# Optimization experiments

Measured on AMD Instinct MI355X. Metric: run time of the kernel, lower is better.

Reference implementation:

```python
import jax, jax.numpy as jnp
import numpy as np

# --- static config (matches init_kwargs) ---
B, S, DIM = 1, 2048, 1024
H, G, DK, DV = 16, 4, 64, 64
HPG = H // G
L, D, LSEL, NSEL, W = 32, 16, 64, 16, 512
NCMP = (S - L) // D + 1            # number of compressed blocks over full prefill
J = S // LSEL                      # number of selection blocks
GH = 32                            # gate hidden
NEG = -1e30


def rope(x, pos):
    # x: [B, S, N, Dh]; llama-style half rotation
    Dh = x.shape[-1]
    inv = 1.0 / (10000.0 ** (np.arange(0, Dh, 2) / Dh))
    ang = pos[:, None] * inv[None, :]                      # [S, Dh/2]
    cos = jnp.asarray(np.cos(ang), jnp.float32)[None, :, None, :]
    sin = jnp.asarray(np.sin(ang), jnp.float32)[None, :, None, :]
    x1, x2 = jnp.split(x, 2, axis=-1)
    return jnp.concatenate([x1 * cos - x2 * sin, x2 * cos + x1 * sin], axis=-1)


def masked_softmax(s, m):
    p = jax.nn.softmax(jnp.where(m, s, NEG), axis=-1)
    # rows with no visible keys produce 0 output (empty attention)
    return jnp.where(jnp.any(m, axis=-1, keepdims=True), p, 0.0)


def setup_inputs() -> dict:
    key = jax.random.key(0)
    ks = jax.random.split(key, 12)
    def w(k, shape, fan):
        return jax.random.normal(k, shape, jnp.float32) / np.sqrt(fan)
    return {
        'x': jax.random.normal(ks[0], (B, S, DIM), jnp.float32),
        'W_Q': w(ks[1], (DIM, H * DK), DIM),
        'W_K_sel': w(ks[2], (DIM, G * DK), DIM),
        'W_V_sel': w(ks[3], (DIM, G * DV), DIM),
        'W_K_win': w(ks[4], (DIM, G * DK), DIM),
        'W_V_win': w(ks[5], (DIM, G * DV), DIM),
        'W_K_cmp': w(ks[6], (DIM, G * DK), DIM),
        'W_V_cmp': w(ks[7], (DIM, G * DV), DIM),
        'W_out': w(ks[8], (H * DV, DIM), H * DV),
        'gate_w1': w(ks[9], (DK, GH), DK),
        'gate_b1': jnp.zeros((GH,), jnp.float32),
        'gate_w2': 0.1 * jax.random.normal(ks[10], (GH, 3), jnp.float32),
        'gate_b2': jnp.zeros((3,), jnp.float32),
    }


def reference(x, W_Q, W_K_sel, W_V_sel, W_K_win, W_V_win, W_K_cmp, W_V_cmp,
              W_out, gate_w1, gate_b1, gate_w2, gate_b2):
    pos = np.arange(S)
    s_ = np.arange(S)
    scale = 1.0 / np.sqrt(DK)

    Q = rope((x @ W_Q).reshape(B, S, H, DK), pos).reshape(B, S, G, HPG, DK)

    def proj_kv(Wk, Wv):
        K = rope((x @ Wk).reshape(B, S, G, DK), pos).transpose(0, 2, 1, 3)  # [B,G,S,Dk]
        V = (x @ Wv).reshape(B, S, G, DV).transpose(0, 2, 1, 3)            # [B,G,S,Dv]
        return K, V

    K_sel, V_sel = proj_kv(W_K_sel, W_V_sel)
    K_win, V_win = proj_kv(W_K_win, W_V_win)
    K_cr, V_cr = proj_kv(W_K_cmp, W_V_cmp)

    # --- compressed branch: avg-pool (len L, stride D) of roped K / raw V ---
    bidx = np.arange(NCMP)[:, None] * D + np.arange(L)[None, :]   # [NCMP, L]
    K_cmp = K_cr[:, :, bidx].mean(axis=3)                         # [B,G,NCMP,Dk]
    V_cmp = V_cr[:, :, bidx].mean(axis=3)
    vis_c = (np.arange(NCMP)[None, :] * D + L) <= (s_[:, None] + 1)  # block fully in past
    sc_c = jnp.einsum('bsghd,bgcd->bsghc', Q, K_cmp) * scale
    p_cmp = masked_softmax(sc_c, jnp.asarray(vis_c)[None, :, None, None, :])
    O_cmp = jnp.einsum('bsghc,bgce->bsghe', p_cmp, V_cmp)

    # --- map compressed probs -> selection-block scores (overlap fractions) ---
    i0 = np.arange(NCMP)[:, None] * D
    j0 = np.arange(J)[None, :] * LSEL
    ov = np.maximum(0, np.minimum(i0 + L, j0 + LSEL) - np.maximum(i0, j0)) / L
    p_grp = jnp.einsum('bsghc,cj->bsgj', p_cmp, jnp.asarray(ov, np.float32))  # sum over heads in group

    vis_j = (np.arange(J)[None, :] * LSEL) <= s_[:, None]
    forced = (np.arange(J)[None, :] == 0) | (np.arange(J)[None, :] == (s_ // LSEL)[:, None])
    score = jnp.where(jnp.asarray(vis_j)[None, :, None, :], p_grp, NEG)
    score = jnp.where(jnp.asarray(forced)[None, :, None, :], 1e9, score)  # force block 0 + current block
    topj = jax.lax.top_k(score, NSEL)[1]                                   # [B,S,G,NSEL]
    blk = jax.nn.one_hot(topj, J, dtype=jnp.float32).sum(axis=-2) > 0      # [B,S,G,J]

    tok2blk = np.repeat(np.arange(J), LSEL)[:S]
    causal = s_[:, None] >= s_[None, :]                                    # u <= t
    sel_mask = blk[:, :, :, tok2blk] & jnp.asarray(causal)[None, :, None, :]  # [B,S,G,S]
    sc_s = jnp.einsum('bsghd,bgud->bsghu', Q, K_sel) * scale
    O_sel = jnp.einsum('bsghu,bgue->bsghe',
                       masked_softmax(sc_s, sel_mask[:, :, :, None, :]), V_sel)

    # --- sliding window branch ---
    win_mask = causal & (s_[None, :] > s_[:, None] - W)
    sc_w = jnp.einsum('bsghd,bgud->bsghu', Q, K_win) * scale
    O_win = jnp.einsum('bsghu,bgue->bsghe',
                       masked_softmax(sc_w, jnp.asarray(win_mask)[None, :, None, None, :]), V_win)

    # --- gating MLP on head-pooled query per group ---
    gl = jax.nn.silu(Q.mean(axis=3) @ gate_w1 + gate_b1) @ gate_w2 + gate_b2  # [B,S,G,3]
    pg = jax.nn.softmax(gl, axis=-1)
    t2 = jax.lax.top_k(gl, 2)[0]
    peaked = (t2[..., 0] - t2[..., 1]) > 50.0
    gates = jnp.where(peaked[..., None],
                      jax.nn.one_hot(jnp.argmax(gl, axis=-1), 3, dtype=gl.dtype), pg)

    O = (gates[..., 0, None, None] * O_cmp
         + gates[..., 1, None, None] * O_sel
         + gates[..., 2, None, None] * O_win)          # [B,S,G,h,Dv]
    return O.reshape(B, S, H * DV) @ W_out
```

## Files before the change

### kernel.cpp

```cpp
#include <hip/hip_runtime.h>
#include <math.h>

#define S 2048
#define DIM 1024
#define H 16
#define G 4
#define HPG 4
#define DK 64
#define DV 64
#define NCMP 127
#define JBLK 32
#define NSEL 16
#define WWIN 512
#define GH 32
#define SCL2 0.18033688011112042f

typedef __attribute__((ext_vector_type(8))) __bf16 bf16x8;
typedef __attribute__((ext_vector_type(4))) float f32x4;

__device__ __forceinline__ unsigned short f2bf(float f) {
  unsigned u = __float_as_uint(f);
  unsigned r = (u + 0x7FFFu + ((u >> 16) & 1u)) >> 16;
  return (unsigned short)r;
}

__device__ __forceinline__ unsigned short f2bf_hw(float f) {
  __bf16 b = (__bf16)f;
  return *(unsigned short*)&b;
}

__device__ __forceinline__ float bf2f(unsigned short u) {
  return __uint_as_float((unsigned)u << 16);
}

__device__ __forceinline__ f32x4 mfma16(bf16x8 a, bf16x8 b, f32x4 c) {
  return __builtin_amdgcn_mfma_f32_16x16x32_bf16(a, b, c, 0, 0, 0);
}

__global__ void rope_table(float* __restrict__ cosT, float* __restrict__ sinT) {
  int idx = blockIdx.x * blockDim.x + threadIdx.x;
  if (idx >= S * 32) return;
  int s = idx >> 5, i = idx & 31;
  double inv = pow(10000.0, -2.0 * (double)i / 64.0);
  double ang = (double)s * inv;
  cosT[idx] = (float)cos(ang);
  sinT[idx] = (float)sin(ang);
}

__device__ __forceinline__ void gemm_body_k(const float* __restrict__ A,
                                            const float* __restrict__ B,
                                            float* __restrict__ C,
                                            int N, int K, int bm, int bn,
                                            int kS, int kE,
                                            float* As , float* Bs ) {
  int tid = threadIdx.x;
  int tr = tid >> 4, tc = tid & 15;
  float acc[4][4] = {{0.f}};
  int arow = tid >> 2;
  int kba = (tid & 3) << 3;
  int brow = tid >> 4;
  int bcol = (tid & 15) << 2;
  const float* Ab = A + (size_t)(bm * 64) * K;
  const float* Bb = B + bn * 64;

  float4 a0 = *(const float4*)(Ab + (size_t)arow * K + kS + kba);
  float4 a1 = *(const float4*)(Ab + (size_t)arow * K + kS + kba + 4);
  float4 b0 = *(const float4*)(Bb + (size_t)(kS + brow) * N + bcol);
  float4 b1 = *(const float4*)(Bb + (size_t)(kS + brow + 16) * N + bcol);

  for (int k0 = kS; k0 < kE; k0 += 32) {
    __syncthreads();
    {
      float av[8] = {a0.x, a0.y, a0.z, a0.w, a1.x, a1.y, a1.z, a1.w};
#pragma unroll
      for (int i = 0; i < 8; ++i) {
        int k = kba + i;
        As[k * 64 + (arow ^ (((k >> 3) & 3) << 3))] = av[i];
      }
      *(float4*)&Bs[brow * 64 + bcol] = b0;
      *(float4*)&Bs[(brow + 16) * 64 + bcol] = b1;
    }
    __syncthreads();
    if (k0 + 32 < kE) {
      a0 = *(const float4*)(Ab + (size_t)arow * K + k0 + 32 + kba);
      a1 = *(const float4*)(Ab + (size_t)arow * K + k0 + 32 + kba + 4);
      b0 = *(const float4*)(Bb + (size_t)(k0 + 32 + brow) * N + bcol);
      b1 = *(const float4*)(Bb + (size_t)(k0 + 32 + brow + 16) * N + bcol);
    }
#pragma unroll
    for (int kk = 0; kk < 32; ++kk) {
      float4 a = *(const float4*)&As[kk * 64 + ((tr << 2) ^ (((kk >> 3) & 3) << 3))];
      float4 b = *(const float4*)&Bs[kk * 64 + (tc << 2)];
      acc[0][0] += a.x * b.x; acc[0][1] += a.x * b.y; acc[0][2] += a.x * b.z; acc[0][3] += a.x * b.w;
      acc[1][0] += a.y * b.x; acc[1][1] += a.y * b.y; acc[1][2] += a.y * b.z; acc[1][3] += a.y * b.w;
      acc[2][0] += a.z * b.x; acc[2][1] += a.z * b.y; acc[2][2] += a.z * b.z; acc[2][3] += a.z * b.w;
      acc[3][0] += a.w * b.x; acc[3][1] += a.w * b.y; acc[3][2] += a.w * b.z; acc[3][3] += a.w * b.w;
    }
  }
  for (int i = 0; i < 4; ++i)
    for (int jj = 0; jj < 4; ++jj)
      C[(size_t)(bm * 64 + (tr << 2) + i) * N + bn * 64 + (tc << 2) + jj] = acc[i][jj];
}

__device__ __forceinline__ void proj_body(
    const unsigned short* __restrict__ xb, const unsigned short* __restrict__ Wt,
    const float* __restrict__ cosT, const float* __restrict__ sinT,
    unsigned short* __restrict__ Kb_s, unsigned short* __restrict__ Vt_s,
    unsigned short* __restrict__ Kb_w, unsigned short* __restrict__ Vt_w,
    unsigned short* __restrict__ Vt_c,
    int s0, int g, int mat, unsigned short* xs, unsigned short* ws) {
  int tid = threadIdx.x, w = tid >> 6, lane = tid & 63;
  int l15 = lane & 15, lg = lane >> 4;
  int rswz = (l15 & 7) << 3;
  bool isV = (mat == 1) || (mat == 3) || (mat == 4);
  const unsigned short* wt = Wt + ((size_t)mat * 256 + g * 64) * 1024;

  f32x4 acc[4];
#pragma unroll
  for (int nt = 0; nt < 4; ++nt) acc[nt] = (f32x4){0.f, 0.f, 0.f, 0.f};

  for (int k0 = 0; k0 < DIM; k0 += 64) {
#pragma unroll
    for (int e = 0; e < 2; ++e) {
      int flat = tid + e * 256;
      int row = flat >> 3, cc = flat & 7;
      int dsti = row * 64 + ((cc ^ (row & 7)) << 3);
      *(float4*)&xs[dsti] = *(const float4*)(xb + (size_t)(s0 + row) * DIM + k0 + cc * 8);
      *(float4*)&ws[dsti] = *(const float4*)(wt + (size_t)row * DIM + k0 + cc * 8);
    }
    __syncthreads();
    const unsigned short* aP = isV ? ws : xs;
    const unsigned short* bP = isV ? xs : ws;
    int arow = w * 16 + l15;
    bf16x8 af[2];
#pragma unroll
    for (int kc = 0; kc < 2; ++kc)
      af[kc] = *(const bf16x8*)&aP[(arow * 64 + kc * 32 + lg * 8) ^ rswz];
#pragma unroll
    for (int nt = 0; nt < 4; ++nt) {
      int brow = nt * 16 + l15;
      bf16x8 b0 = *(const bf16x8*)&bP[(brow * 64 + lg * 8) ^ rswz];
      bf16x8 b1 = *(const bf16x8*)&bP[(brow * 64 + 32 + lg * 8) ^ rswz];
      acc[nt] = mfma16(af[0], b0, acc[nt]);
      acc[nt] = mfma16(af[1], b1, acc[nt]);
    }
    __syncthreads();
  }

  if (!isV) {
    unsigned short* Kb = (mat == 0) ? Kb_s : Kb_w;
#pragma unroll
    for (int rr = 0; rr < 4; ++rr) {
      int tok = s0 + w * 16 + lg * 4 + rr;
#pragma unroll
      for (int p = 0; p < 2; ++p) {
        int i = p * 16 + l15;
        float c = cosT[tok * 32 + i], sn = sinT[tok * 32 + i];
        float x1 = acc[p][rr], x2 = acc[p + 2][rr];
        Kb[((size_t)g * S + tok) * 64 + i] = f2bf(x1 * c - x2 * sn);
        Kb[((size_t)g * S + tok) * 64 + i + 32] = f2bf(x2 * c + x1 * sn);
      }
    }
  } else {
    unsigned short* Vt = (mat == 1) ? Vt_s : (mat == 3) ? Vt_w : Vt_c;
#pragma unroll
    for (int rr = 0; rr < 4; ++rr) {
      int col = w * 16 + lg * 4 + rr;
#pragma unroll
      for (int nt = 0; nt < 4; ++nt) {
        int tok = s0 + nt * 16 + l15;
        Vt[((size_t)g * 64 + col) * S + tok] = f2bf(acc[nt][rr]);
      }
    }
  }
}

__global__ __launch_bounds__(256) void qk_proj(
    const float* __restrict__ x, const float* __restrict__ W_Q,
    const float* __restrict__ W_Kc, float* __restrict__ Pq, float* __restrict__ Pk,
    const unsigned short* __restrict__ xb, const unsigned short* __restrict__ Wt,
    const float* __restrict__ cosT, const float* __restrict__ sinT,
    unsigned short* __restrict__ Kb_s, unsigned short* __restrict__ Vt_s,
    unsigned short* __restrict__ Kb_w, unsigned short* __restrict__ Vt_w,
    unsigned short* __restrict__ Vt_c) {
  __shared__ __align__(16) float lds_f[4096];
  int bid = blockIdx.x;
  int r = bid % 3;
  if (r < 2) {
    int gid = (bid / 3) * 2 + r;
    int z = gid / 640;
    int rem = gid % 640;
    int ct = rem % 20;
    int bm = rem / 20;
    int kS = z * 512, kE = kS + 512;
    float* As = lds_f;
    float* Bs = lds_f + 2048;
    if (ct < 16)
      gemm_body_k(x, W_Q, Pq + (size_t)z * S * 1024, 1024, DIM, bm, ct, kS, kE, As, Bs);
    else
      gemm_body_k(x, W_Kc, Pk + (size_t)z * S * 256, 256, DIM, bm, ct - 16, kS, kE, As, Bs);
  } else {
    int pid = bid / 3;
    int s0b = pid % 32;
    int g = (pid / 32) % 4;
    int mat = pid / 128;
    unsigned short* xs = (unsigned short*)lds_f;
    unsigned short* ws = xs + 4096;
    proj_body(xb, Wt, cosT, sinT, Kb_s, Vt_s, Kb_w, Vt_w, Vt_c, s0b * 64, g, mat,
              xs, ws);
  }
}

__global__ __launch_bounds__(256) void reduce_rope(
    const float* __restrict__ Pq, const float* __restrict__ Pk,
    const float* __restrict__ cosT, const float* __restrict__ sinT,
    float* __restrict__ Qb, unsigned short* __restrict__ Qbf,
    float* __restrict__ Kcr) {
  int idx = blockIdx.x * 256 + threadIdx.x;
  const int NQ = S * H * 32;
  if (idx < NQ) {
    int i = idx & 31;
    int rest = idx >> 5;
    int h = rest & 15;
    int s = rest >> 4;
    size_t base = (size_t)s * 1024 + h * 64 + i;
    float a1 = Pq[base] + Pq[(size_t)S * 1024 + base];
    float a2 = Pq[base + 32] + Pq[(size_t)S * 1024 + base + 32];
    float c = cosT[s * 32 + i], sn = sinT[s * 32 + i];
    float q1 = a1 * c - a2 * sn, q2 = a2 * c + a1 * sn;
    Qb[base] = q1;
    Qb[base + 32] = q2;
    Qbf[base] = f2bf(q1);
    Qbf[base + 32] = f2bf(q2);
  } else {
    int j = idx - NQ;
    if (j >= S * G * 32) return;
    int i = j & 31;
    int rest = j >> 5;
    int g = rest & 3;
    int s = rest >> 2;
    size_t base = (size_t)s * 256 + g * 64 + i;
    float a1 = Pk[base] + Pk[(size_t)S * 256 + base];
    float a2 = Pk[base + 32] + Pk[(size_t)S * 256 + base + 32];
    float c = cosT[s * 32 + i], sn = sinT[s * 32 + i];
    Kcr[base] = a1 * c - a2 * sn;
    Kcr[base + 32] = a2 * c + a1 * sn;
  }
}

__global__ __launch_bounds__(256) void fconv(const float* __restrict__ a,
                                             unsigned short* __restrict__ b) {
  int idx = (blockIdx.x * 256 + threadIdx.x) * 8;
  float4 x = *(const float4*)&a[idx];
  float4 y = *(const float4*)&a[idx + 4];
  union { unsigned short us[8]; float4 f4; } t;
  t.us[0] = f2bf(x.x); t.us[1] = f2bf(x.y); t.us[2] = f2bf(x.z); t.us[3] = f2bf(x.w);
  t.us[4] = f2bf(y.x); t.us[5] = f2bf(y.y); t.us[6] = f2bf(y.z); t.us[7] = f2bf(y.w);
  *(float4*)&b[idx] = t.f4;
}

__global__ __launch_bounds__(256) void wtrans(const float* __restrict__ W0,
                                              const float* __restrict__ W1,
                                              const float* __restrict__ W2,
                                              const float* __restrict__ W3,
                                              const float* __restrict__ W4,
                                              unsigned short* __restrict__ Wt) {
  __shared__ float t[64][65];
  int k0 = blockIdx.x * 64;
  int n0 = blockIdx.y * 64;
  int m = blockIdx.z;
  const float* W = (m == 0) ? W0 : (m == 1) ? W1 : (m == 2) ? W2 : (m == 3) ? W3 : W4;
  int tid = threadIdx.x;
  int rr = tid >> 4, c4 = (tid & 15) * 4;
#pragma unroll
  for (int e = 0; e < 4; ++e) {
    int row = rr + e * 16;
    float4 v = *(const float4*)(W + (size_t)(k0 + row) * 256 + n0 + c4);
    t[c4 + 0][row] = v.x;
    t[c4 + 1][row] = v.y;
    t[c4 + 2][row] = v.z;
    t[c4 + 3][row] = v.w;
  }
  __syncthreads();
#pragma unroll
  for (int e = 0; e < 2; ++e) {
    int flat = tid + e * 256;
    int col = flat >> 3, kc = (flat & 7) * 8;
    union { unsigned short us[8]; float4 f4; } u;
#pragma unroll
    for (int i = 0; i < 8; ++i) u.us[i] = f2bf(t[col][kc + i]);
    *(float4*)(Wt + ((size_t)m * 256 + n0 + col) * 1024 + k0 + kc) = u.f4;
  }
}

__global__ __launch_bounds__(256) void wtrans_o(const float* __restrict__ W,
                                                unsigned short* __restrict__ Wt) {
  __shared__ float t[64][65];
  int k0 = blockIdx.x * 64;
  int n0 = blockIdx.y * 64;
  int tid = threadIdx.x;
  int rr = tid >> 4, c4 = (tid & 15) * 4;
#pragma unroll
  for (int e = 0; e < 4; ++e) {
    int row = rr + e * 16;
    float4 v = *(const float4*)(W + (size_t)(k0 + row) * 1024 + n0 + c4);
    t[c4 + 0][row] = v.x;
    t[c4 + 1][row] = v.y;
    t[c4 + 2][row] = v.z;
    t[c4 + 3][row] = v.w;
  }
  __syncthreads();
#pragma unroll
  for (int e = 0; e < 2; ++e) {
    int flat = tid + e * 256;
    int col = flat >> 3, kc = (flat & 7) * 8;
    union { unsigned short us[8]; float4 f4; } u;
#pragma unroll
    for (int i = 0; i < 8; ++i) u.us[i] = f2bf(t[col][kc + i]);
    *(float4*)(Wt + (size_t)(n0 + col) * 1024 + k0 + kc) = u.f4;
  }
}

__global__ __launch_bounds__(256) void gemm_out(const unsigned short* __restrict__ Ob,
                                                const unsigned short* __restrict__ Wt,
                                                float* __restrict__ out) {
  __shared__ unsigned short xs[64 * 64];
  __shared__ unsigned short ws[64 * 64];
  int s0 = blockIdx.x * 64;
  int n0 = blockIdx.y * 64;
  int tid = threadIdx.x, w = tid >> 6, lane = tid & 63;
  int l15 = lane & 15, lg = lane >> 4;
  int rswz = (l15 & 7) << 3;

  f32x4 acc[4];
#pragma unroll
  for (int nt = 0; nt < 4; ++nt) acc[nt] = (f32x4){0.f, 0.f, 0.f, 0.f};

  for (int k0 = 0; k0 < DIM; k0 += 64) {
#pragma unroll
    for (int e = 0; e < 2; ++e) {
      int flat = tid + e * 256;
      int row = flat >> 3, cc = flat & 7;
      int dsti = row * 64 + ((cc ^ (row & 7)) << 3);
      *(float4*)&xs[dsti] = *(const float4*)(Ob + (size_t)(s0 + row) * DIM + k0 + cc * 8);
      *(float4*)&ws[dsti] = *(const float4*)(Wt + (size_t)(n0 + row) * DIM + k0 + cc * 8);
    }
    __syncthreads();
    int arow = w * 16 + l15;
    bf16x8 af0 = *(const bf16x8*)&xs[(arow * 64 + lg * 8) ^ rswz];
    bf16x8 af1 = *(const bf16x8*)&xs[(arow * 64 + 32 + lg * 8) ^ rswz];
#pragma unroll
    for (int nt = 0; nt < 4; ++nt) {
      int brow = nt * 16 + l15;
      bf16x8 b0 = *(const bf16x8*)&ws[(brow * 64 + lg * 8) ^ rswz];
      bf16x8 b1 = *(const bf16x8*)&ws[(brow * 64 + 32 + lg * 8) ^ rswz];
      acc[nt] = mfma16(af0, b0, acc[nt]);
      acc[nt] = mfma16(af1, b1, acc[nt]);
    }
    __syncthreads();
  }

#pragma unroll
  for (int nt = 0; nt < 4; ++nt)
#pragma unroll
    for (int rr = 0; rr < 4; ++rr)
      out[(size_t)(s0 + w * 16 + lg * 4 + rr) * 1024 + n0 + nt * 16 + l15] =
          acc[nt][rr];
}

__global__ void pool_cmp(const float* __restrict__ Kcr,
                         const unsigned short* __restrict__ Vtc,
                         float* __restrict__ Kc, float* __restrict__ Vc) {
  int c = blockIdx.x, g = blockIdx.y, d = threadIdx.x;
  float sk = 0.f, sv = 0.f;
  const unsigned short* vrow = Vtc + ((size_t)g * 64 + d) * S + c * 16;
  for (int l = 0; l < 32; ++l) {
    sk += Kcr[(size_t)((c * 16 + l) * G + g) * 64 + d];
    sv += bf2f(vrow[l]);
  }
  Kc[(size_t)(g * NCMP + c) * 64 + d] = sk * (1.f / 32.f);
  Vc[(size_t)(g * NCMP + c) * 64 + d] = sv * (1.f / 32.f);
}

__device__ __forceinline__ void cmp_body(const float* __restrict__ Q,
                                         const float* __restrict__ Kc,
                                         const float* __restrict__ Vc,
                                         float* __restrict__ Ocmp,
                                         unsigned int* __restrict__ selm,
                                         int s, int g,
                                         float* q4 , float* sc ,
                                         float* pg ) {
  int tid = threadIdx.x;
  int nvis = (s >= 31) ? (((s - 31) >> 4) + 1) : 0;
  {
    int h = tid >> 6, d = tid & 63;
    q4[h * 64 + d] = Q[(size_t)(s * H + g * HPG + h) * 64 + d];
  }
  __syncthreads();

  if (tid < 128) {
    int c = tid;
    if (c < nvis) {
      float a0 = 0.f, a1 = 0.f, a2 = 0.f, a3 = 0.f;
      const float* kr = &Kc[(size_t)(g * NCMP + c) * 64];
#pragma unroll 4
      for (int kk = 0; kk < 16; ++kk) {
        float4 kv = *(const float4*)&kr[kk * 4];
        float4 q0 = *(const float4*)&q4[0 * 64 + kk * 4];
        float4 q1 = *(const float4*)&q4[1 * 64 + kk * 4];
        float4 q2 = *(const float4*)&q4[2 * 64 + kk * 4];
        float4 q3 = *(const float4*)&q4[3 * 64 + kk * 4];
        a0 += q0.x * kv.x + q0.y * kv.y + q0.z * kv.z + q0.w * kv.w;
        a1 += q1.x * kv.x + q1.y * kv.y + q1.z * kv.z + q1.w * kv.w;
        a2 += q2.x * kv.x + q2.y * kv.y + q2.z * kv.z + q2.w * kv.w;
        a3 += q3.x * kv.x + q3.y * kv.y + q3.z * kv.z + q3.w * kv.w;
      }
      sc[0 * 128 + c] = a0 * 0.125f;
      sc[1 * 128 + c] = a1 * 0.125f;
      sc[2 * 128 + c] = a2 * 0.125f;
      sc[3 * 128 + c] = a3 * 0.125f;
    } else {
      sc[0 * 128 + c] = -INFINITY;
      sc[1 * 128 + c] = -INFINITY;
      sc[2 * 128 + c] = -INFINITY;
      sc[3 * 128 + c] = -INFINITY;
    }
  }
  __syncthreads();

  int w = tid >> 6, lane = tid & 63;
  {
    float v0 = sc[w * 128 + lane];
    float v1 = (lane + 64 < NCMP) ? sc[w * 128 + lane + 64] : -INFINITY;
    float m = fmaxf(v0, v1);
    for (int off = 32; off; off >>= 1) m = fmaxf(m, __shfl_xor(m, off));
    float e0 = (m > -INFINITY && v0 > -INFINITY) ? expf(v0 - m) : 0.f;
    float e1 = (m > -INFINITY && v1 > -INFINITY) ? expf(v1 - m) : 0.f;
    float sum = e0 + e1;
    for (int off = 32; off; off >>= 1) sum += __shfl_xor(sum, off);
    float inv = (sum > 0.f) ? 1.f / sum : 0.f;
    sc[w * 128 + lane] = e0 * inv;
    if (lane + 64 < NCMP) sc[w * 128 + lane + 64] = e1 * inv;
    if (lane == 63) sc[w * 128 + 127] = 0.f;
  }
  __syncthreads();

  {
    int h = tid >> 6, d = tid & 63;
    float o = 0.f;
#pragma unroll 4
    for (int c = 0; c < nvis; ++c)
      o += sc[h * 128 + c] * Vc[(size_t)(g * NCMP + c) * 64 + d];
    Ocmp[(size_t)(s * H + g * HPG + h) * 64 + d] = o;
  }

  if (tid < JBLK) {
    int j = tid;
    float a = 0.f;
#pragma unroll
    for (int h = 0; h < 4; ++h) {
      const float* row = &sc[h * 128];
      float v = row[4 * j] + row[4 * j + 1] + row[4 * j + 2] + 0.5f * row[4 * j + 3];
      if (j > 0) v += 0.5f * row[4 * j - 1];
      a += v;
    }
    pg[j] = a;
  }
  __syncthreads();

  if (tid < 64) {
    int j = tid & 31;
    int cur = s >> 6;
    float v = (j * 64 <= s) ? pg[j] : -1e30f;
    if (j == 0 || j == cur) v = 1e9f;
    unsigned int mask = 0;
#pragma unroll 1
    for (int n = 0; n < NSEL; ++n) {
      float bv = v;
      int bj = j;
#pragma unroll
      for (int off = 1; off < 32; off <<= 1) {
        float ov = __shfl_xor(bv, off);
        int oj = __shfl_xor(bj, off);
        if (ov > bv || (ov == bv && oj < bj)) { bv = ov; bj = oj; }
      }
      mask |= 1u << bj;
      if (j == bj) v = -INFINITY;
    }
    if (tid == 0) selm[(size_t)s * G + g] = mask;
  }
}

template <int MODE>
__device__ __forceinline__ void attn_body(
    const unsigned short* __restrict__ Qbf, const unsigned short* __restrict__ Kb,
    const unsigned short* __restrict__ Vtb, const unsigned int* __restrict__ selm,
    float* __restrict__ O, int t0, int g,
    unsigned short* Kl, unsigned short* Vt, unsigned short* Pl,
    unsigned int* sel_l, int* blist, int* nB_p) {
  int tid = threadIdx.x;
  int w = tid >> 6, lane = tid & 63;
  int l15 = lane & 15, lg = lane >> 4;
  int rswz = (l15 & 7) << 3;
  int jdiag = t0 >> 6;

  if (MODE == 0 && tid < 16) sel_l[tid] = selm[(t0 + tid) * G + g];
  __syncthreads();
  if (tid == 0) {
    int n = 0;
    if (MODE == 0) {
      unsigned int un = 0;
      for (int i = 0; i < 16; ++i) un |= sel_l[i];
      for (int j = 0; j <= jdiag; ++j)
        if ((un >> j) & 1u) blist[n++] = j;
    } else {
      int lo = t0 - (WWIN - 1);
      int j0 = (lo > 0) ? (lo >> 6) : 0;
      for (int j = j0; j <= jdiag; ++j) blist[n++] = j;
    }
    *nB_p = n;
  }
  __syncthreads();
  int nB = *nB_p;

  int tok = t0 + l15;
  bf16x8 qf[2];
  {
    const unsigned short* qb = Qbf + ((size_t)tok * H + g * HPG + w) * 64;
    qf[0] = *(const bf16x8*)(qb + lg * 8);
    qf[1] = *(const bf16x8*)(qb + 32 + lg * 8);
  }

  float mrun = -INFINITY, lrun = 0.f;
  f32x4 oacc[4];
#pragma unroll
  for (int dt = 0; dt < 4; ++dt) oacc[dt] = (f32x4){0.f, 0.f, 0.f, 0.f};

  for (int b = 0; b < nB; ++b) {
    int j = blist[b];
    int ku = j * 64;

    {
      const unsigned short* src = Kb + ((size_t)g * S + ku) * 64;
#pragma unroll
      for (int c2 = 0; c2 < 2; ++c2) {
        int chunk = tid + c2 * 256;
        int key = chunk >> 3, cc = chunk & 7;
        *(float4*)&Kl[key * 64 + ((cc ^ (key & 7)) << 3)] =
            *(const float4*)(src + chunk * 8);
      }
#pragma unroll
      for (int c2 = 0; c2 < 2; ++c2) {
        int chunk = tid + c2 * 256;
        int dim = chunk >> 3, cc = chunk & 7;
        *(float4*)&Vt[dim * 64 + ((cc ^ (dim & 7)) << 3)] =
            *(const float4*)(Vtb + ((size_t)g * 64 + dim) * S + ku + cc * 8);
      }
    }
    __syncthreads();

    f32x4 sf[4];
#pragma unroll
    for (int kt = 0; kt < 4; ++kt) sf[kt] = (f32x4){0.f, 0.f, 0.f, 0.f};
#pragma unroll
    for (int kt = 0; kt < 4; ++kt) {
      int krow = kt * 16 + l15;
      bf16x8 kf0 = *(const bf16x8*)&Kl[(krow * 64 + lg * 8) ^ rswz];
      bf16x8 kf1 = *(const bf16x8*)&Kl[(krow * 64 + 32 + lg * 8) ^ rswz];
      sf[kt] = mfma16(kf0, qf[0], sf[kt]);
      sf[kt] = mfma16(kf1, qf[1], sf[kt]);
    }

    bool bsel = true;
    if (MODE == 0) bsel = ((sel_l[l15] >> j) & 1u) != 0;
    float sv2[4][4];
    if (j == jdiag) {
#pragma unroll
      for (int kt = 0; kt < 4; ++kt)
#pragma unroll
        for (int rr = 0; rr < 4; ++rr) {
          int u = ku + kt * 16 + lg * 4 + rr;
          sv2[kt][rr] = (u <= tok) ? sf[kt][rr] * SCL2 : -INFINITY;
        }
    } else if (MODE == 1 && (ku + WWIN <= t0 + 15)) {
#pragma unroll
      for (int kt = 0; kt < 4; ++kt)
#pragma unroll
        for (int rr = 0; rr < 4; ++rr) {
          int u = ku + kt * 16 + lg * 4 + rr;
          sv2[kt][rr] = (u + WWIN > tok) ? sf[kt][rr] * SCL2 : -INFINITY;
        }
    } else {
#pragma unroll
      for (int kt = 0; kt < 4; ++kt)
#pragma unroll
        for (int rr = 0; rr < 4; ++rr) sv2[kt][rr] = sf[kt][rr] * SCL2;
    }

    float pmax = -INFINITY;
#pragma unroll
    for (int kt = 0; kt < 4; ++kt)
#pragma unroll
      for (int rr = 0; rr < 4; ++rr) pmax = fmaxf(pmax, sv2[kt][rr]);
    pmax = fmaxf(pmax, __shfl_xor(pmax, 16));
    pmax = fmaxf(pmax, __shfl_xor(pmax, 32));
    if (MODE == 0 && !bsel) pmax = -INFINITY;

    if (__any(pmax > mrun)) {
      float mnew = fmaxf(mrun, pmax);
      float mc = (mnew == -INFINITY) ? 0.f : mnew;
      float fac = exp2f(mrun - mc);
      mrun = mnew;
      lrun *= fac;
#pragma unroll
      for (int dt = 0; dt < 4; ++dt)
#pragma unroll
        for (int rr = 0; rr < 4; ++rr) oacc[dt][rr] *= fac;
    }
    float mcb = (MODE == 0 && !bsel) ? INFINITY
                                     : ((mrun == -INFINITY) ? 0.f : mrun);

    float psum = 0.f;
    unsigned short pb[16];
#pragma unroll
    for (int kt = 0; kt < 4; ++kt)
#pragma unroll
      for (int rr = 0; rr < 4; ++rr) {
        float e = exp2f(sv2[kt][rr] - mcb);
        psum += e;
        pb[kt * 4 + rr] = f2bf_hw(e);
      }
    psum += __shfl_xor(psum, 16);
    psum += __shfl_xor(psum, 32);
    lrun += psum;

    {
      unsigned short* pw = Pl + w * 1024;
#pragma unroll
      for (int kt = 0; kt < 4; ++kt) {
        int idx = (l15 * 64 + kt * 16 + lg * 4) ^ rswz;
        unsigned int lo = (unsigned)pb[kt * 4] | ((unsigned)pb[kt * 4 + 1] << 16);
        unsigned int hi = (unsigned)pb[kt * 4 + 2] | ((unsigned)pb[kt * 4 + 3] << 16);
        *(uint2*)&pw[idx] = make_uint2(lo, hi);
      }
    }

#pragma unroll
    for (int kc = 0; kc < 2; ++kc) {
      bf16x8 pf = *(const bf16x8*)&Pl[w * 1024 + ((l15 * 64 + kc * 32 + lg * 8) ^ rswz)];
#pragma unroll
      for (int dt = 0; dt < 4; ++dt) {
        bf16x8 vf = *(const bf16x8*)&Vt[((dt * 16 + l15) * 64 + kc * 32 + lg * 8) ^ rswz];
        oacc[dt] = mfma16(vf, pf, oacc[dt]);
      }
    }
    __syncthreads();
  }

  {
    float inv = (lrun > 0.f) ? 1.f / lrun : 0.f;
    float* ob = O + ((size_t)tok * H + g * HPG + w) * 64;
#pragma unroll
    for (int dt = 0; dt < 4; ++dt) {
      float4 v;
      v.x = oacc[dt][0] * inv;
      v.y = oacc[dt][1] * inv;
      v.z = oacc[dt][2] * inv;
      v.w = oacc[dt][3] * inv;
      *(float4*)(ob + dt * 16 + lg * 4) = v;
    }
  }
}

__global__ __launch_bounds__(256) void cmp_win(
    const float* __restrict__ Qb, const float* __restrict__ Kc,
    const float* __restrict__ Vc, float* __restrict__ Ocmp,
    unsigned int* __restrict__ selm, const unsigned short* __restrict__ Qbf,
    const unsigned short* __restrict__ Kbw, const unsigned short* __restrict__ Vtw,
    float* __restrict__ Owin) {
  __shared__ __align__(16) unsigned char ldsb[24832];
  int bid = blockIdx.x;
  if (bid % 17 != 16) {
    int cid = (bid / 17) * 16 + (bid % 17);
    int s = cid >> 2, g = cid & 3;
    float* q4 = (float*)ldsb;
    float* sc = q4 + 256;
    float* pg = sc + 512;
    cmp_body(Qb, Kc, Vc, Ocmp, selm, s, g, q4, sc, pg);
  } else {
    int pid = bid / 17;
    int t0 = (pid & 127) * 16;
    int g = pid >> 7;
    unsigned short* Kl = (unsigned short*)ldsb;
    unsigned short* Vt = Kl + 4096;
    unsigned short* Pl = Vt + 4096;
    int* blist = (int*)(Pl + 4096);
    int* nB_p = blist + JBLK;
    attn_body<1>(Qbf, Kbw, Vtw, nullptr, Owin, t0, g, Kl, Vt, Pl, nullptr, blist,
                 nB_p);
  }
}

__global__ __launch_bounds__(256) void attn_sel(
    const unsigned short* __restrict__ Qbf, const unsigned short* __restrict__ Kbs,
    const unsigned short* __restrict__ Vts, const unsigned int* __restrict__ selm,
    float* __restrict__ Osel) {
  __shared__ unsigned short Kl[4096];
  __shared__ unsigned short Vt[4096];
  __shared__ unsigned short Pl[4096];
  __shared__ unsigned int sel_l[16];
  __shared__ int blist[JBLK];
  __shared__ int nB_s;
  int t0 = blockIdx.x * 16;
  int g = blockIdx.y;
  attn_body<0>(Qbf, Kbs, Vts, selm, Osel, t0, g, Kl, Vt, Pl, sel_l, blist, &nB_s);
}

__global__ void gate_kernel(const float* __restrict__ Q, const float* __restrict__ w1,
                            const float* __restrict__ b1, const float* __restrict__ w2,
                            const float* __restrict__ b2, float* __restrict__ gates) {
  int idx = blockIdx.x * blockDim.x + threadIdx.x;
  if (idx >= S * G) return;
  int s = idx >> 2, g = idx & 3;
  float qm[64];
#pragma unroll
  for (int d = 0; d < 64; ++d) {
    float a = 0.f;
    for (int hp = 0; hp < HPG; ++hp) a += Q[(size_t)(s * H + g * HPG + hp) * 64 + d];
    qm[d] = a * 0.25f;
  }
  float gl[3] = {b2[0], b2[1], b2[2]};
  for (int j = 0; j < GH; ++j) {
    float z = b1[j];
    for (int d = 0; d < 64; ++d) z += qm[d] * w1[d * GH + j];
    float sl = z / (1.f + expf(-z));
    gl[0] += sl * w2[j * 3 + 0];
    gl[1] += sl * w2[j * 3 + 1];
    gl[2] += sl * w2[j * 3 + 2];
  }
  float m = fmaxf(gl[0], fmaxf(gl[1], gl[2]));
  float e0 = expf(gl[0] - m), e1 = expf(gl[1] - m), e2 = expf(gl[2] - m);
  float inv = 1.f / (e0 + e1 + e2);
  float p0 = e0 * inv, p1 = e1 * inv, p2 = e2 * inv;
  int am = (gl[0] >= gl[1] && gl[0] >= gl[2]) ? 0 : ((gl[1] >= gl[2]) ? 1 : 2);
  float t1 = (am == 0) ? fmaxf(gl[1], gl[2]) : ((am == 1) ? fmaxf(gl[0], gl[2]) : fmaxf(gl[0], gl[1]));
  if (m - t1 > 50.f) {
    p0 = (am == 0) ? 1.f : 0.f;
    p1 = (am == 1) ? 1.f : 0.f;
    p2 = (am == 2) ? 1.f : 0.f;
  }
  gates[idx * 3 + 0] = p0;
  gates[idx * 3 + 1] = p1;
  gates[idx * 3 + 2] = p2;
}

__global__ void combine(const float* __restrict__ Oc, const float* __restrict__ Os,
                        const float* __restrict__ Ow, const float* __restrict__ gates,
                        unsigned short* __restrict__ Ob) {
  int idx = blockIdx.x * blockDim.x + threadIdx.x;
  if (idx >= S * H * DV) return;
  int h = (idx >> 6) & 15;
  int s = idx >> 10;
  int g = h >> 2;
  const float* gp = &gates[(size_t)(s * G + g) * 3];
  Ob[idx] = f2bf(gp[0] * Oc[idx] + gp[1] * Os[idx] + gp[2] * Ow[idx]);
}

extern "C" void kernel_launch(void* const* d_in, const int* in_sizes, int n_in,
                              void* d_out, int out_size, void* d_ws, size_t ws_size,
                              hipStream_t stream) {
  const float* x = (const float*)d_in[0];
  const float* W_Q = (const float*)d_in[1];
  const float* W_K_sel = (const float*)d_in[2];
  const float* W_V_sel = (const float*)d_in[3];
  const float* W_K_win = (const float*)d_in[4];
  const float* W_V_win = (const float*)d_in[5];
  const float* W_K_cmp = (const float*)d_in[6];
  const float* W_V_cmp = (const float*)d_in[7];
  const float* W_out = (const float*)d_in[8];
  const float* gw1 = (const float*)d_in[9];
  const float* gb1 = (const float*)d_in[10];
  const float* gw2 = (const float*)d_in[11];
  const float* gb2 = (const float*)d_in[12];

  float* w = (float*)d_ws;
  float* cosT = w;  w += S * 32;
  float* sinT = w;  w += S * 32;
  float* Qb   = w;  w += S * H * DK;
  float* Kcr  = w;  w += S * G * DK;
  float* Kc   = w;  w += G * NCMP * DK;
  float* Vc   = w;  w += G * NCMP * DV;
  float* Ocmp = w;  w += S * H * DV;
  float* Osel = w;  w += S * H * DV;
  float* Owin = w;  w += S * H * DV;
  float* gates= w;  w += S * G * 3;
  unsigned int* selm = (unsigned int*)w;  w += S * G;
  unsigned short* Kbf_s = (unsigned short*)w;  w += (size_t)G * S * 64 / 2;
  unsigned short* Kbf_w = (unsigned short*)w;  w += (size_t)G * S * 64 / 2;
  unsigned short* Vt_s  = (unsigned short*)w;  w += (size_t)G * S * 64 / 2;
  unsigned short* Vt_w  = (unsigned short*)w;  w += (size_t)G * S * 64 / 2;
  unsigned short* Vt_c  = (unsigned short*)w;  w += (size_t)G * S * 64 / 2;
  unsigned short* Qbf   = (unsigned short*)w;  w += (size_t)S * H * 64 / 2;
  unsigned short* xb    = (unsigned short*)w;  w += (size_t)S * DIM / 2;
  unsigned short* Wt    = (unsigned short*)w;  w += (size_t)5 * 256 * DIM / 2;
  unsigned short* Ob    = (unsigned short*)w;  w += (size_t)S * H * DV / 2;
  unsigned short* WtO   = (unsigned short*)w;  w += (size_t)DIM * DIM / 2;

  float* Pq = Ocmp;
  float* Pk = Owin;

  rope_table<<<(S * 32 + 255) / 256, 256, 0, stream>>>(cosT, sinT);
  fconv<<<(S * DIM) / 2048, 256, 0, stream>>>(x, xb);
  wtrans<<<dim3(DIM / 64, 4, 5), 256, 0, stream>>>(W_K_sel, W_V_sel, W_K_win,
                                                   W_V_win, W_V_cmp, Wt);
  wtrans_o<<<dim3(DIM / 64, DIM / 64), 256, 0, stream>>>(W_out, WtO);

  qk_proj<<<1920, 256, 0, stream>>>(x, W_Q, W_K_cmp, Pq, Pk, xb, Wt, cosT, sinT,
                                    Kbf_s, Vt_s, Kbf_w, Vt_w, Vt_c);
  reduce_rope<<<(S * (H + G) * 32) / 256, 256, 0, stream>>>(Pq, Pk, cosT, sinT,
                                                            Qb, Qbf, Kcr);

  pool_cmp<<<dim3(NCMP, G), 64, 0, stream>>>(Kcr, Vt_c, Kc, Vc);

  cmp_win<<<8704, 256, 0, stream>>>(Qb, Kc, Vc, Ocmp, selm, Qbf, Kbf_w, Vt_w, Owin);
  attn_sel<<<dim3(S / 16, G), 256, 0, stream>>>(Qbf, Kbf_s, Vt_s, selm, Osel);

  gate_kernel<<<(S * G + 255) / 256, 256, 0, stream>>>(Qb, gw1, gb1, gw2, gb2, gates);
  combine<<<(S * H * DV + 255) / 256, 256, 0, stream>>>(Ocmp, Osel, Owin, gates, Ob);

  gemm_out<<<dim3(S / 64, DIM / 64), 256, 0, stream>>>(Ob, WtO, (float*)d_out);
}
```

Baseline: 328.6 us.

## Merge prep kernels, fuse pooling with gating, regroup attention launches

Folds the rope table, activation conversion and both weight transposes into one prep launch with block-range dispatch. Compressed-KV pooling and the gating MLP now share one post_reduce launch. The compressed attention gets its own launch, and selection and window attention are merged into one 3D launch instead of interleaving window work with compressed blocks. The aim is fewer launches and better balance between attention branches, at the cost of losing overlap between compressed and window work within a single launch.

```diff
diff --git a/kernel.cpp b/kernel.cpp
--- a/kernel.cpp
+++ b/kernel.cpp
@@ -37,14 +37,82 @@
   return __builtin_amdgcn_mfma_f32_16x16x32_bf16(a, b, c, 0, 0, 0);
 }
 
-__global__ void rope_table(float* __restrict__ cosT, float* __restrict__ sinT) {
-  int idx = blockIdx.x * blockDim.x + threadIdx.x;
-  if (idx >= S * 32) return;
-  int s = idx >> 5, i = idx & 31;
-  double inv = pow(10000.0, -2.0 * (double)i / 64.0);
-  double ang = (double)s * inv;
-  cosT[idx] = (float)cos(ang);
-  sinT[idx] = (float)sin(ang);
+__global__ __launch_bounds__(256) void prep(
+    const float* __restrict__ x, const float* __restrict__ W0,
+    const float* __restrict__ W1, const float* __restrict__ W2,
+    const float* __restrict__ W3, const float* __restrict__ W4,
+    const float* __restrict__ W_out, float* __restrict__ cosT,
+    float* __restrict__ sinT, unsigned short* __restrict__ xb,
+    unsigned short* __restrict__ Wt, unsigned short* __restrict__ WtO) {
+  __shared__ float t[64 * 65];
+  int bid = blockIdx.x, tid = threadIdx.x;
+  if (bid < 256) {
+    int idx = bid * 256 + tid;
+    int s = idx >> 5, i = idx & 31;
+    double inv = pow(10000.0, -2.0 * (double)i / 64.0);
+    double ang = (double)s * inv;
+    cosT[idx] = (float)cos(ang);
+    sinT[idx] = (float)sin(ang);
+  } else if (bid < 1280) {
+    int idx = ((bid - 256) * 256 + tid) * 8;
+    float4 a = *(const float4*)&x[idx];
+    float4 b = *(const float4*)&x[idx + 4];
+    union { unsigned short us[8]; float4 f4; } u;
+    u.us[0] = f2bf(a.x); u.us[1] = f2bf(a.y); u.us[2] = f2bf(a.z); u.us[3] = f2bf(a.w);
+    u.us[4] = f2bf(b.x); u.us[5] = f2bf(b.y); u.us[6] = f2bf(b.z); u.us[7] = f2bf(b.w);
+    *(float4*)&xb[idx] = u.f4;
+  } else if (bid < 1600) {
+    int p = bid - 1280;
+    int m = p / 64;
+    int rem = p % 64;
+    int k0 = (rem & 15) * 64;
+    int n0 = (rem >> 4) * 64;
+    const float* W = (m == 0) ? W0 : (m == 1) ? W1 : (m == 2) ? W2 : (m == 3) ? W3 : W4;
+    int rr = tid >> 4, c4 = (tid & 15) * 4;
+#pragma unroll
+    for (int e = 0; e < 4; ++e) {
+      int row = rr + e * 16;
+      float4 v = *(const float4*)(W + (size_t)(k0 + row) * 256 + n0 + c4);
+      t[(c4 + 0) * 65 + row] = v.x;
+      t[(c4 + 1) * 65 + row] = v.y;
+      t[(c4 + 2) * 65 + row] = v.z;
+      t[(c4 + 3) * 65 + row] = v.w;
+    }
+    __syncthreads();
+#pragma unroll
+    for (int e = 0; e < 2; ++e) {
+      int flat = tid + e * 256;
+      int col = flat >> 3, kc = (flat & 7) * 8;
+      union { unsigned short us[8]; float4 f4; } u;
+#pragma unroll
+      for (int i = 0; i < 8; ++i) u.us[i] = f2bf(t[col * 65 + kc + i]);
+      *(float4*)(Wt + ((size_t)m * 256 + n0 + col) * 1024 + k0 + kc) = u.f4;
+    }
+  } else {
+    int p = bid - 1600;
+    int k0 = (p & 15) * 64;
+    int n0 = (p >> 4) * 64;
+    int rr = tid >> 4, c4 = (tid & 15) * 4;
+#pragma unroll
+    for (int e = 0; e < 4; ++e) {
+      int row = rr + e * 16;
+      float4 v = *(const float4*)(W_out + (size_t)(k0 + row) * 1024 + n0 + c4);
+      t[(c4 + 0) * 65 + row] = v.x;
+      t[(c4 + 1) * 65 + row] = v.y;
+      t[(c4 + 2) * 65 + row] = v.z;
+      t[(c4 + 3) * 65 + row] = v.w;
+    }
+    __syncthreads();
+#pragma unroll
+    for (int e = 0; e < 2; ++e) {
+      int flat = tid + e * 256;
+      int col = flat >> 3, kc = (flat & 7) * 8;
+      union { unsigned short us[8]; float4 f4; } u;
+#pragma unroll
+      for (int i = 0; i < 8; ++i) u.us[i] = f2bf(t[col * 65 + kc + i]);
+      *(float4*)(WtO + (size_t)(n0 + col) * 1024 + k0 + kc) = u.f4;
+    }
+  }
 }
 
 __device__ __forceinline__ void gemm_body_k(const float* __restrict__ A,
@@ -248,138 +316,61 @@
   }
 }
 
-__global__ __launch_bounds__(256) void fconv(const float* __restrict__ a,
-                                             unsigned short* __restrict__ b) {
-  int idx = (blockIdx.x * 256 + threadIdx.x) * 8;
-  float4 x = *(const float4*)&a[idx];
-  float4 y = *(const float4*)&a[idx + 4];
-  union { unsigned short us[8]; float4 f4; } t;
-  t.us[0] = f2bf(x.x); t.us[1] = f2bf(x.y); t.us[2] = f2bf(x.z); t.us[3] = f2bf(x.w);
-  t.us[4] = f2bf(y.x); t.us[5] = f2bf(y.y); t.us[6] = f2bf(y.z); t.us[7] = f2bf(y.w);
-  *(float4*)&b[idx] = t.f4;
-}
-
-__global__ __launch_bounds__(256) void wtrans(const float* __restrict__ W0,
-                                              const float* __restrict__ W1,
-                                              const float* __restrict__ W2,
-                                              const float* __restrict__ W3,
-                                              const float* __restrict__ W4,
-                                              unsigned short* __restrict__ Wt) {
-  __shared__ float t[64][65];
-  int k0 = blockIdx.x * 64;
-  int n0 = blockIdx.y * 64;
-  int m = blockIdx.z;
-  const float* W = (m == 0) ? W0 : (m == 1) ? W1 : (m == 2) ? W2 : (m == 3) ? W3 : W4;
-  int tid = threadIdx.x;
-  int rr = tid >> 4, c4 = (tid & 15) * 4;
-#pragma unroll
-  for (int e = 0; e < 4; ++e) {
-    int row = rr + e * 16;
-    float4 v = *(const float4*)(W + (size_t)(k0 + row) * 256 + n0 + c4);
-    t[c4 + 0][row] = v.x;
-    t[c4 + 1][row] = v.y;
-    t[c4 + 2][row] = v.z;
-    t[c4 + 3][row] = v.w;
-  }
-  __syncthreads();
-#pragma unroll
-  for (int e = 0; e < 2; ++e) {
-    int flat = tid + e * 256;
-    int col = flat >> 3, kc = (flat & 7) * 8;
-    union { unsigned short us[8]; float4 f4; } u;
-#pragma unroll
-    for (int i = 0; i < 8; ++i) u.us[i] = f2bf(t[col][kc + i]);
-    *(float4*)(Wt + ((size_t)m * 256 + n0 + col) * 1024 + k0 + kc) = u.f4;
-  }
-}
-
-__global__ __launch_bounds__(256) void wtrans_o(const float* __restrict__ W,
-                                                unsigned short* __restrict__ Wt) {
-  __shared__ float t[64][65];
-  int k0 = blockIdx.x * 64;
-  int n0 = blockIdx.y * 64;
-  int tid = threadIdx.x;
-  int rr = tid >> 4, c4 = (tid & 15) * 4;
-#pragma unroll
-  for (int e = 0; e < 4; ++e) {
-    int row = rr + e * 16;
-    float4 v = *(const float4*)(W + (size_t)(k0 + row) * 1024 + n0 + c4);
-    t[c4 + 0][row] = v.x;
-    t[c4 + 1][row] = v.y;
-    t[c4 + 2][row] = v.z;
-    t[c4 + 3][row] = v.w;
-  }
-  __syncthreads();
-#pragma unroll
-  for (int e = 0; e < 2; ++e) {
-    int flat = tid + e * 256;
-    int col = flat >> 3, kc = (flat & 7) * 8;
-    union { unsigned short us[8]; float4 f4; } u;
-#pragma unroll
-    for (int i = 0; i < 8; ++i) u.us[i] = f2bf(t[col][kc + i]);
-    *(float4*)(Wt + (size_t)(n0 + col) * 1024 + k0 + kc) = u.f4;
-  }
-}
-
-__global__ __launch_bounds__(256) void gemm_out(const unsigned short* __restrict__ Ob,
-                                                const unsigned short* __restrict__ Wt,
-                                                float* __restrict__ out) {
-  __shared__ unsigned short xs[64 * 64];
-  __shared__ unsigned short ws[64 * 64];
-  int s0 = blockIdx.x * 64;
-  int n0 = blockIdx.y * 64;
-  int tid = threadIdx.x, w = tid >> 6, lane = tid & 63;
-  int l15 = lane & 15, lg = lane >> 4;
-  int rswz = (l15 & 7) << 3;
-
-  f32x4 acc[4];
-#pragma unroll
-  for (int nt = 0; nt < 4; ++nt) acc[nt] = (f32x4){0.f, 0.f, 0.f, 0.f};
-
-  for (int k0 = 0; k0 < DIM; k0 += 64) {
-#pragma unroll
-    for (int e = 0; e < 2; ++e) {
-      int flat = tid + e * 256;
-      int row = flat >> 3, cc = flat & 7;
-      int dsti = row * 64 + ((cc ^ (row & 7)) << 3);
-      *(float4*)&xs[dsti] = *(const float4*)(Ob + (size_t)(s0 + row) * DIM + k0 + cc * 8);
-      *(float4*)&ws[dsti] = *(const float4*)(Wt + (size_t)(n0 + row) * DIM + k0 + cc * 8);
-    }
-    __syncthreads();
-    int arow = w * 16 + l15;
-    bf16x8 af0 = *(const bf16x8*)&xs[(arow * 64 + lg * 8) ^ rswz];
-    bf16x8 af1 = *(const bf16x8*)&xs[(arow * 64 + 32 + lg * 8) ^ rswz];
-#pragma unroll
-    for (int nt = 0; nt < 4; ++nt) {
-      int brow = nt * 16 + l15;
-      bf16x8 b0 = *(const bf16x8*)&ws[(brow * 64 + lg * 8) ^ rswz];
-      bf16x8 b1 = *(const bf16x8*)&ws[(brow * 64 + 32 + lg * 8) ^ rswz];
-      acc[nt] = mfma16(af0, b0, acc[nt]);
-      acc[nt] = mfma16(af1, b1, acc[nt]);
-    }
-    __syncthreads();
-  }
-
-#pragma unroll
-  for (int nt = 0; nt < 4; ++nt)
-#pragma unroll
-    for (int rr = 0; rr < 4; ++rr)
-      out[(size_t)(s0 + w * 16 + lg * 4 + rr) * 1024 + n0 + nt * 16 + l15] =
-          acc[nt][rr];
-}
-
-__global__ void pool_cmp(const float* __restrict__ Kcr,
-                         const unsigned short* __restrict__ Vtc,
-                         float* __restrict__ Kc, float* __restrict__ Vc) {
-  int c = blockIdx.x, g = blockIdx.y, d = threadIdx.x;
-  float sk = 0.f, sv = 0.f;
-  const unsigned short* vrow = Vtc + ((size_t)g * 64 + d) * S + c * 16;
-  for (int l = 0; l < 32; ++l) {
-    sk += Kcr[(size_t)((c * 16 + l) * G + g) * 64 + d];
-    sv += bf2f(vrow[l]);
-  }
-  Kc[(size_t)(g * NCMP + c) * 64 + d] = sk * (1.f / 32.f);
-  Vc[(size_t)(g * NCMP + c) * 64 + d] = sv * (1.f / 32.f);
+__global__ __launch_bounds__(256) void post_reduce(
+    const float* __restrict__ Kcr, const unsigned short* __restrict__ Vtc,
+    float* __restrict__ Kc, float* __restrict__ Vc, const float* __restrict__ Q,
+    const float* __restrict__ w1, const float* __restrict__ b1,
+    const float* __restrict__ w2, const float* __restrict__ b2,
+    float* __restrict__ gates) {
+  int bid = blockIdx.x, tid = threadIdx.x;
+  if (bid < 127) {
+    int item = bid * 256 + tid;
+    int c = item >> 8;
+    int g = (item >> 6) & 3;
+    int d = item & 63;
+    float sk = 0.f, sv = 0.f;
+    const unsigned short* vrow = Vtc + ((size_t)g * 64 + d) * S + c * 16;
+    for (int l = 0; l < 32; ++l) {
+      sk += Kcr[(size_t)((c * 16 + l) * G + g) * 64 + d];
+      sv += bf2f(vrow[l]);
+    }
+    Kc[(size_t)(g * NCMP + c) * 64 + d] = sk * (1.f / 32.f);
+    Vc[(size_t)(g * NCMP + c) * 64 + d] = sv * (1.f / 32.f);
+  } else {
+    int idx = (bid - 127) * 256 + tid;
+    int s = idx >> 2, g = idx & 3;
+    float qm[64];
+#pragma unroll
+    for (int d = 0; d < 64; ++d) {
+      float a = 0.f;
+      for (int hp = 0; hp < HPG; ++hp) a += Q[(size_t)(s * H + g * HPG + hp) * 64 + d];
+      qm[d] = a * 0.25f;
+    }
+    float gl[3] = {b2[0], b2[1], b2[2]};
+    for (int j = 0; j < GH; ++j) {
+      float z = b1[j];
+      for (int d = 0; d < 64; ++d) z += qm[d] * w1[d * GH + j];
+      float sl = z / (1.f + expf(-z));
+      gl[0] += sl * w2[j * 3 + 0];
+      gl[1] += sl * w2[j * 3 + 1];
+      gl[2] += sl * w2[j * 3 + 2];
+    }
+    float m = fmaxf(gl[0], fmaxf(gl[1], gl[2]));
+    float e0 = expf(gl[0] - m), e1 = expf(gl[1] - m), e2 = expf(gl[2] - m);
+    float inv = 1.f / (e0 + e1 + e2);
+    float p0 = e0 * inv, p1 = e1 * inv, p2 = e2 * inv;
+    int am = (gl[0] >= gl[1] && gl[0] >= gl[2]) ? 0 : ((gl[1] >= gl[2]) ? 1 : 2);
+    float t1 = (am == 0) ? fmaxf(gl[1], gl[2])
+                         : ((am == 1) ? fmaxf(gl[0], gl[2]) : fmaxf(gl[0], gl[1]));
+    if (m - t1 > 50.f) {
+      p0 = (am == 0) ? 1.f : 0.f;
+      p1 = (am == 1) ? 1.f : 0.f;
+      p2 = (am == 2) ? 1.f : 0.f;
+    }
+    gates[idx * 3 + 0] = p0;
+    gates[idx * 3 + 1] = p1;
+    gates[idx * 3 + 2] = p2;
+  }
 }
 
 __device__ __forceinline__ void cmp_body(const float* __restrict__ Q,
@@ -388,8 +379,7 @@
                                          float* __restrict__ Ocmp,
                                          unsigned int* __restrict__ selm,
                                          int s, int g,
-                                         float* q4 , float* sc ,
-                                         float* pg ) {
+                                         float* q4, float* sc, float* pg) {
   int tid = threadIdx.x;
   int nvis = (s >= 31) ? (((s - 31) >> 4) + 1) : 0;
   {
@@ -491,6 +481,17 @@
   }
 }
 
+__global__ __launch_bounds__(256) void cmp_attn(const float* __restrict__ Qb,
+                                                const float* __restrict__ Kc,
+                                                const float* __restrict__ Vc,
+                                                float* __restrict__ Ocmp,
+                                                unsigned int* __restrict__ selm) {
+  __shared__ float q4[256];
+  __shared__ float sc[512];
+  __shared__ float pg[JBLK];
+  cmp_body(Qb, Kc, Vc, Ocmp, selm, blockIdx.x, blockIdx.y, q4, sc, pg);
+}
+
 template <int MODE>
 __device__ __forceinline__ void attn_body(
     const unsigned short* __restrict__ Qbf, const unsigned short* __restrict__ Kb,
@@ -672,39 +673,12 @@
   }
 }
 
-__global__ __launch_bounds__(256) void cmp_win(
-    const float* __restrict__ Qb, const float* __restrict__ Kc,
-    const float* __restrict__ Vc, float* __restrict__ Ocmp,
-    unsigned int* __restrict__ selm, const unsigned short* __restrict__ Qbf,
+__global__ __launch_bounds__(256) void attn_fused(
+    const unsigned short* __restrict__ Qbf,
+    const unsigned short* __restrict__ Kbs, const unsigned short* __restrict__ Vts,
     const unsigned short* __restrict__ Kbw, const unsigned short* __restrict__ Vtw,
-    float* __restrict__ Owin) {
-  __shared__ __align__(16) unsigned char ldsb[24832];
-  int bid = blockIdx.x;
-  if (bid % 17 != 16) {
-    int cid = (bid / 17) * 16 + (bid % 17);
-    int s = cid >> 2, g = cid & 3;
-    float* q4 = (float*)ldsb;
-    float* sc = q4 + 256;
-    float* pg = sc + 512;
-    cmp_body(Qb, Kc, Vc, Ocmp, selm, s, g, q4, sc, pg);
-  } else {
-    int pid = bid / 17;
-    int t0 = (pid & 127) * 16;
-    int g = pid >> 7;
-    unsigned short* Kl = (unsigned short*)ldsb;
-    unsigned short* Vt = Kl + 4096;
-    unsigned short* Pl = Vt + 4096;
-    int* blist = (int*)(Pl + 4096);
-    int* nB_p = blist + JBLK;
-    attn_body<1>(Qbf, Kbw, Vtw, nullptr, Owin, t0, g, Kl, Vt, Pl, nullptr, blist,
-                 nB_p);
-  }
-}
-
-__global__ __launch_bounds__(256) void attn_sel(
-    const unsigned short* __restrict__ Qbf, const unsigned short* __restrict__ Kbs,
-    const unsigned short* __restrict__ Vts, const unsigned int* __restrict__ selm,
-    float* __restrict__ Osel) {
+    const unsigned int* __restrict__ selm,
+    float* __restrict__ Osel, float* __restrict__ Owin) {
   __shared__ unsigned short Kl[4096];
   __shared__ unsigned short Vt[4096];
   __shared__ unsigned short Pl[4096];
@@ -713,45 +687,11 @@
   __shared__ int nB_s;
   int t0 = blockIdx.x * 16;
   int g = blockIdx.y;
-  attn_body<0>(Qbf, Kbs, Vts, selm, Osel, t0, g, Kl, Vt, Pl, sel_l, blist, &nB_s);
-}
-
-__global__ void gate_kernel(const float* __restrict__ Q, const float* __restrict__ w1,
-                            const float* __restrict__ b1, const float* __restrict__ w2,
-                            const float* __restrict__ b2, float* __restrict__ gates) {
-  int idx = blockIdx.x * blockDim.x + threadIdx.x;
-  if (idx >= S * G) return;
-  int s = idx >> 2, g = idx & 3;
-  float qm[64];
-#pragma unroll
-  for (int d = 0; d < 64; ++d) {
-    float a = 0.f;
-    for (int hp = 0; hp < HPG; ++hp) a += Q[(size_t)(s * H + g * HPG + hp) * 64 + d];
-    qm[d] = a * 0.25f;
-  }
-  float gl[3] = {b2[0], b2[1], b2[2]};
-  for (int j = 0; j < GH; ++j) {
-    float z = b1[j];
-    for (int d = 0; d < 64; ++d) z += qm[d] * w1[d * GH + j];
-    float sl = z / (1.f + expf(-z));
-    gl[0] += sl * w2[j * 3 + 0];
-    gl[1] += sl * w2[j * 3 + 1];
-    gl[2] += sl * w2[j * 3 + 2];
-  }
-  float m = fmaxf(gl[0], fmaxf(gl[1], gl[2]));
-  float e0 = expf(gl[0] - m), e1 = expf(gl[1] - m), e2 = expf(gl[2] - m);
-  float inv = 1.f / (e0 + e1 + e2);
-  float p0 = e0 * inv, p1 = e1 * inv, p2 = e2 * inv;
-  int am = (gl[0] >= gl[1] && gl[0] >= gl[2]) ? 0 : ((gl[1] >= gl[2]) ? 1 : 2);
-  float t1 = (am == 0) ? fmaxf(gl[1], gl[2]) : ((am == 1) ? fmaxf(gl[0], gl[2]) : fmaxf(gl[0], gl[1]));
-  if (m - t1 > 50.f) {
-    p0 = (am == 0) ? 1.f : 0.f;
-    p1 = (am == 1) ? 1.f : 0.f;
-    p2 = (am == 2) ? 1.f : 0.f;
-  }
-  gates[idx * 3 + 0] = p0;
-  gates[idx * 3 + 1] = p1;
-  gates[idx * 3 + 2] = p2;
+  if (blockIdx.z == 0)
+    attn_body<0>(Qbf, Kbs, Vts, selm, Osel, t0, g, Kl, Vt, Pl, sel_l, blist, &nB_s);
+  else
+    attn_body<1>(Qbf, Kbw, Vtw, nullptr, Owin, t0, g, Kl, Vt, Pl, sel_l, blist,
+                 &nB_s);
 }
 
 __global__ void combine(const float* __restrict__ Oc, const float* __restrict__ Os,
@@ -764,6 +704,53 @@
   int g = h >> 2;
   const float* gp = &gates[(size_t)(s * G + g) * 3];
   Ob[idx] = f2bf(gp[0] * Oc[idx] + gp[1] * Os[idx] + gp[2] * Ow[idx]);
+}
+
+__global__ __launch_bounds__(256) void gemm_out(const unsigned short* __restrict__ Ob,
+                                                const unsigned short* __restrict__ Wt,
+                                                float* __restrict__ out) {
+  __shared__ unsigned short xs[64 * 64];
+  __shared__ unsigned short ws[64 * 64];
+  int s0 = blockIdx.x * 64;
+  int n0 = blockIdx.y * 64;
+  int tid = threadIdx.x, w = tid >> 6, lane = tid & 63;
+  int l15 = lane & 15, lg = lane >> 4;
+  int rswz = (l15 & 7) << 3;
+
+  f32x4 acc[4];
+#pragma unroll
+  for (int nt = 0; nt < 4; ++nt) acc[nt] = (f32x4){0.f, 0.f, 0.f, 0.f};
+
+  for (int k0 = 0; k0 < DIM; k0 += 64) {
+#pragma unroll
+    for (int e = 0; e < 2; ++e) {
+      int flat = tid + e * 256;
+      int row = flat >> 3, cc = flat & 7;
+      int dsti = row * 64 + ((cc ^ (row & 7)) << 3);
+      *(float4*)&xs[dsti] = *(const float4*)(Ob + (size_t)(s0 + row) * DIM + k0 + cc * 8);
+      *(float4*)&ws[dsti] = *(const float4*)(Wt + (size_t)(n0 + row) * DIM + k0 + cc * 8);
+    }
+    __syncthreads();
+    int arow = w * 16 + l15;
+    bf16x8 af0 = *(const bf16x8*)&xs[(arow * 64 + lg * 8) ^ rswz];
+    bf16x8 af1 = *(const bf16x8*)&xs[(arow * 64 + 32 + lg * 8) ^ rswz];
+#pragma unroll
+    for (int nt = 0; nt < 4; ++nt) {
+      int brow = nt * 16 + l15;
+      bf16x8 b0 = *(const bf16x8*)&ws[(brow * 64 + lg * 8) ^ rswz];
+      bf16x8 b1 = *(const bf16x8*)&ws[(brow * 64 + 32 + lg * 8) ^ rswz];
+      acc[nt] = mfma16(af0, b0, acc[nt]);
+      acc[nt] = mfma16(af1, b1, acc[nt]);
+    }
+    __syncthreads();
+  }
+
+#pragma unroll
+  for (int nt = 0; nt < 4; ++nt)
+#pragma unroll
+    for (int rr = 0; rr < 4; ++rr)
+      out[(size_t)(s0 + w * 16 + lg * 4 + rr) * 1024 + n0 + nt * 16 + l15] =
+          acc[nt][rr];
 }
 
 extern "C" void kernel_launch(void* const* d_in, const int* in_sizes, int n_in,
@@ -809,23 +796,21 @@
   float* Pq = Ocmp;
   float* Pk = Owin;
 
-  rope_table<<<(S * 32 + 255) / 256, 256, 0, stream>>>(cosT, sinT);
-  fconv<<<(S * DIM) / 2048, 256, 0, stream>>>(x, xb);
-  wtrans<<<dim3(DIM / 64, 4, 5), 256, 0, stream>>>(W_K_sel, W_V_sel, W_K_win,
-                                                   W_V_win, W_V_cmp, Wt);
-  wtrans_o<<<dim3(DIM / 64, DIM / 64), 256, 0, stream>>>(W_out, WtO);
+  prep<<<1856, 256, 0, stream>>>(x, W_K_sel, W_V_sel, W_K_win, W_V_win, W_V_cmp,
+                                 W_out, cosT, sinT, xb, Wt, WtO);
 
   qk_proj<<<1920, 256, 0, stream>>>(x, W_Q, W_K_cmp, Pq, Pk, xb, Wt, cosT, sinT,
                                     Kbf_s, Vt_s, Kbf_w, Vt_w, Vt_c);
-  reduce_rope<<<(S * (H + G) * 32) / 256, 256, 0, stream>>>(Pq, Pk, cosT, sinT,
-                                                            Qb, Qbf, Kcr);
-
-  pool_cmp<<<dim3(NCMP, G), 64, 0, stream>>>(Kcr, Vt_c, Kc, Vc);
-
-  cmp_win<<<8704, 256, 0, stream>>>(Qb, Kc, Vc, Ocmp, selm, Qbf, Kbf_w, Vt_w, Owin);
-  attn_sel<<<dim3(S / 16, G), 256, 0, stream>>>(Qbf, Kbf_s, Vt_s, selm, Osel);
-
-  gate_kernel<<<(S * G + 255) / 256, 256, 0, stream>>>(Qb, gw1, gb1, gw2, gb2, gates);
+  reduce_rope<<<(S * (H + G) * 32 + 255) / 256, 256, 0, stream>>>(
+      Pq, Pk, cosT, sinT, Qb, Qbf, Kcr);
+
+  post_reduce<<<159, 256, 0, stream>>>(Kcr, Vt_c, Kc, Vc, Qb, gw1, gb1, gw2, gb2,
+                                       gates);
+
+  cmp_attn<<<dim3(S, G), 256, 0, stream>>>(Qb, Kc, Vc, Ocmp, selm);
+  attn_fused<<<dim3(S / 16, G, 2), 256, 0, stream>>>(Qbf, Kbf_s, Vt_s, Kbf_w, Vt_w,
+                                                     selm, Osel, Owin);
+
   combine<<<(S * H * DV + 255) / 256, 256, 0, stream>>>(Ocmp, Osel, Owin, gates, Ob);
 
   gemm_out<<<dim3(S / 64, DIM / 64), 256, 0, stream>>>(Ob, WtO, (float*)d_out);
```

After: 281.7 us, median of 2. 1.17x faster.
